# Performance work log

Hardware: AMD Instinct MI355X
Metric: run time of the kernel (lower is better)

The kernel has to match this reference:

```python
import jax, jax.numpy as jnp
import numpy as np

NUM_HEADS = 16
LN_EPS = 1e-5


def setup_inputs() -> dict:
    key = jax.random.key(0)
    ks = jax.random.split(key, 5)
    B, S, E = 4, 1024, 1024
    x = jax.random.normal(ks[0], (B, S, E), dtype=jnp.float32)
    # Linear weights stored torch-style [out, in]; scaled for stable softmax
    Wq = jax.random.normal(ks[1], (E, E), dtype=jnp.float32) * (E ** -0.5)
    Wk = jax.random.normal(ks[2], (E, E), dtype=jnp.float32) * (E ** -0.5)
    Wv = jax.random.normal(ks[3], (E, E), dtype=jnp.float32) * (E ** -0.5)
    Wo = jax.random.normal(ks[4], (E, E), dtype=jnp.float32) * (E ** -0.5)
    gamma = jnp.ones((E,), dtype=jnp.float32)
    beta = jnp.zeros((E,), dtype=jnp.float32)
    return {"x": x, "Wq": Wq, "Wk": Wk, "Wv": Wv, "Wo": Wo, "gamma": gamma, "beta": beta}


def reference(x, Wq, Wk, Wv, Wo, gamma, beta):
    B, S, E = x.shape
    H = NUM_HEADS
    D = E // H
    scale = 1.0 / (D ** 0.5)

    q = x @ Wq.T                      # [B,S,E]
    k = (x @ Wk.T) * scale            # [B,S,E]
    v = x @ Wv.T                      # [B,S,E]

    qh = q.reshape(B, S, H, D)
    kh = k.reshape(B, S, H, D)
    qk = jnp.einsum('bthd,bshd->bhts', qh, kh)        # [B,H,T,S]

    causal = jnp.tril(jnp.ones((S, S), dtype=bool))   # mask==0 -> -inf
    qk = jnp.where(causal, qk, -jnp.inf)
    attn = jax.nn.softmax(qk, axis=-1)                # [B,H,T,S]

    # Faithful to torch.unflatten(v, dim=2, sizes=[-1, num_heads]):
    # heads are the LAST axis of the value split (transposed vs q/k).
    vh = v.reshape(B, S, D, H)                        # [B,S,D,H]
    # einsum 'kjlm,kmij->kiml': out[b,t,h,d] = sum_s vh[b,s,d,h]*attn[b,h,t,s]
    qkv = jnp.einsum('bsdh,bhts->bthd', vh, attn)     # [B,T,H,D]
    qkv = qkv.reshape(B, S, E)

    # LayerNorm over last dim
    mu = jnp.mean(qkv, axis=-1, keepdims=True)
    var = jnp.mean(jnp.square(qkv - mu), axis=-1, keepdims=True)
    ln = (qkv - mu) * jax.lax.rsqrt(var + LN_EPS) * gamma + beta

    return ln @ Wo.T
```

## Files before the change

### kernel.cpp

```cpp
#include <hip/hip_runtime.h>
#include <stdint.h>


using bf16x8 = __attribute__((ext_vector_type(8))) short;
using f32x4  = __attribute__((ext_vector_type(4))) float;
using u16x8  = __attribute__((ext_vector_type(8))) unsigned short;

#define AS1 __attribute__((address_space(1)))
#define AS3 __attribute__((address_space(3)))

__device__ __forceinline__ void gload16(const void* g, void* l) {
  __builtin_amdgcn_global_load_lds((const AS1 uint32_t*)g, (AS3 uint32_t*)l, 16, 0, 0);
}

__device__ __forceinline__ unsigned short f2bf(float f) {
  union { float f; uint32_t u; } v; v.f = f;
  uint32_t u = v.u + 0x7fffu + ((v.u >> 16) & 1u);
  return (unsigned short)(u >> 16);
}
__device__ __forceinline__ float bf2f(unsigned short h) {
  union { uint32_t u; float f; } v; v.u = ((uint32_t)h) << 16;
  return v.f;
}

__global__ __launch_bounds__(256) void cvt_all(const float* __restrict__ x,
                                               const float* __restrict__ Wq,
                                               const float* __restrict__ Wk,
                                               const float* __restrict__ Wv,
                                               const float* __restrict__ Wo,
                                               unsigned short* __restrict__ xb,
                                               unsigned short* __restrict__ wcat,
                                               unsigned short* __restrict__ wob) {
  int i = (int)blockIdx.x * 256 + (int)threadIdx.x;
  const float* src; unsigned short* dst; int off; float scale = 1.0f;
  if (i < 1048576)      { src = x;  dst = xb;             off = i; }
  else if (i < 1310720) { src = Wq; dst = wcat;           off = i - 1048576; }
  else if (i < 1572864) { src = Wk; dst = wcat + 1048576; off = i - 1310720; scale = 0.125f; }
  else if (i < 1835008) { src = Wv; dst = wcat + 2097152; off = i - 1572864; }
  else                  { src = Wo; dst = wob;            off = i - 1835008; }
  float4 v = reinterpret_cast<const float4*>(src)[off];
  ushort4 o;
  o.x = f2bf(v.x * scale);
  o.y = f2bf(v.y * scale);
  o.z = f2bf(v.z * scale);
  o.w = f2bf(v.w * scale);
  reinterpret_cast<ushort4*>(dst)[off] = o;
}

template<int OUTF32>
__global__ __launch_bounds__(256, 2) void gemm_bt(const unsigned short* __restrict__ A,
                                                  const unsigned short* __restrict__ B,
                                                  void* __restrict__ Cv,
                                                  int M, int N, int K) {
  (void)M;
  __shared__ __align__(16) unsigned short lA[128 * 32];
  __shared__ __align__(16) unsigned short lB[128 * 32];
  const int tn_cnt = N >> 7;
  const int nwg = gridDim.x;
  int bid = (int)blockIdx.x;
  int bid2 = (bid & 7) * (nwg >> 3) + (bid >> 3);
  int tm = bid2 / tn_cnt, tn = bid2 % tn_cnt;
  int t = (int)threadIdx.x;
  int w = t >> 6, lane = t & 63, lr = lane & 15, hi = lane >> 4;
  int wr = w >> 1, wc = w & 1;
  int srow = t >> 2, scol = (t & 3) << 3;
  const unsigned short* a0 = A + (size_t)(tm * 128 + srow) * K + scol;
  const unsigned short* a1 = a0 + (size_t)64 * K;
  const unsigned short* b0 = B + (size_t)(tn * 128 + srow) * K + scol;
  const unsigned short* b1 = b0 + (size_t)64 * K;
  char* dA0 = (char*)lA + w * 1024;
  char* dA1 = (char*)lA + 4096 + w * 1024;
  char* dB0 = (char*)lB + w * 1024;
  char* dB1 = (char*)lB + 4096 + w * 1024;
  f32x4 acc[4][4] = {};
  for (int k0 = 0; k0 < K; k0 += 32) {
    __syncthreads();
    gload16(a0 + k0, dA0);
    gload16(a1 + k0, dA1);
    gload16(b0 + k0, dB0);
    gload16(b1 + k0, dB1);
    __syncthreads();
    bf16x8 af[4], bfr[4];
#pragma unroll
    for (int mi = 0; mi < 4; ++mi)
      af[mi] = *reinterpret_cast<const bf16x8*>(&lA[(wr * 64 + mi * 16 + lr) * 32 + hi * 8]);
#pragma unroll
    for (int ni = 0; ni < 4; ++ni)
      bfr[ni] = *reinterpret_cast<const bf16x8*>(&lB[(wc * 64 + ni * 16 + lr) * 32 + hi * 8]);
#pragma unroll
    for (int mi = 0; mi < 4; ++mi)
#pragma unroll
      for (int ni = 0; ni < 4; ++ni)
        acc[mi][ni] = __builtin_amdgcn_mfma_f32_16x16x32_bf16(af[mi], bfr[ni], acc[mi][ni], 0, 0, 0);
  }
#pragma unroll
  for (int mi = 0; mi < 4; ++mi) {
#pragma unroll
    for (int r = 0; r < 4; ++r) {
      size_t row = (size_t)(tm * 128 + wr * 64 + mi * 16 + hi * 4 + r);
#pragma unroll
      for (int ni = 0; ni < 4; ++ni) {
        int col = tn * 128 + wc * 64 + ni * 16 + lr;
        float v = acc[mi][ni][r];
        if (OUTF32) reinterpret_cast<float*>(Cv)[row * N + col] = v;
        else        reinterpret_cast<unsigned short*>(Cv)[row * N + col] = f2bf(v);
      }
    }
  }
}

__global__ __launch_bounds__(256) void vrepack(const unsigned short* __restrict__ QKV,
                                               unsigned short* __restrict__ VhT) {
  __shared__ __align__(16) unsigned short lT[64 * 72];
  int st = (int)blockIdx.x;
  int ct = (int)blockIdx.y;
  int b  = (int)blockIdx.z;
  int t = (int)threadIdx.x;
#pragma unroll
  for (int i = 0; i < 2; ++i) {
    int c = i * 256 + t;
    int row = c >> 3, ch = c & 7;
    u16x8 v = *reinterpret_cast<const u16x8*>(
        QKV + (size_t)(b * 1024 + st * 64 + row) * 3072 + 2048 + ct * 64 + ch * 8);
    *reinterpret_cast<u16x8*>(&lT[row * 72 + ch * 8]) = v;
  }
  __syncthreads();
#pragma unroll
  for (int i = 0; i < 2; ++i) {
    int c2 = i * 256 + t;
    int cl = c2 >> 3, ch = c2 & 7;
    int h = cl & 15;
    int d = ct * 4 + (cl >> 4);
    u16x8 v;
#pragma unroll
    for (int j = 0; j < 8; ++j) v[j] = lT[(ch * 8 + j) * 72 + cl];
    *reinterpret_cast<u16x8*>(
        VhT + (size_t)((b * 16 + h) * 64 + d) * 1024 + st * 64 + ch * 8) = v;
  }
}

__global__ __launch_bounds__(256, 2) void attn_fwd(const unsigned short* __restrict__ QKV,
                                                   const unsigned short* __restrict__ VhT,
                                                   unsigned short* __restrict__ Out) {
  __shared__ __align__(16) unsigned short lQ[128 * 64];
  __shared__ __align__(16) unsigned short lK[2][64 * 64];
  __shared__ __align__(16) unsigned short lV[2][64 * 64];
  __shared__ __align__(16) unsigned short lP[4][32 * 64];
  int bid = (int)blockIdx.x;
  int half = bid >> 8, idx = bid & 255;
  int bh = idx >> 2, jj = idx & 3;
  int qt = half ? jj : 7 - jj;
  int b = bh >> 4, h = bh & 15;
  int t = (int)threadIdx.x;
  int w = t >> 6, lane = t & 63, lr = lane & 15, hi = lane >> 4;
  (void)lane;

  auto stageKV = [&](int kb, int buf) {
#pragma unroll
    for (int i = 0; i < 2; ++i) {
      int c = i * 256 + t;
      int row = c >> 3, slot = c & 7;
      gload16(QKV + (size_t)(b * 1024 + kb * 64 + row) * 3072 + 1024 + h * 64 + ((slot ^ (row & 7)) << 3),
              (char*)lK + buf * 8192 + i * 4096 + w * 1024);
    }
#pragma unroll
    for (int i = 0; i < 2; ++i) {
      int c = i * 256 + t;
      int row = c >> 3, slot = c & 7;
      gload16(VhT + (size_t)(bh * 64 + row) * 1024 + kb * 64 + ((slot ^ (row & 7)) << 3),
              (char*)lV + buf * 8192 + i * 4096 + w * 1024);
    }
  };

#pragma unroll
  for (int i = 0; i < 4; ++i) {
    int c = i * 256 + t;
    int row = c >> 3, slot = c & 7;
    gload16(QKV + (size_t)(b * 1024 + qt * 128 + row) * 3072 + h * 64 + ((slot ^ (row & 7)) << 3),
            (char*)lQ + i * 4096 + w * 1024);
  }
  stageKV(0, 0);
  __syncthreads();

  bf16x8 qfr[2][2];
#pragma unroll
  for (int qf = 0; qf < 2; ++qf)
#pragma unroll
    for (int kc = 0; kc < 2; ++kc) {
      int row = w * 32 + qf * 16 + lr;
      int slot = (kc * 4 + hi) ^ (row & 7);
      qfr[qf][kc] = *reinterpret_cast<const bf16x8*>((const char*)lQ + row * 128 + slot * 16);
    }
  int qbase = qt * 128 + w * 32;
  f32x4 o[2][4] = {};
  float mrun[2][4], lpart[2][4];
#pragma unroll
  for (int qf = 0; qf < 2; ++qf)
#pragma unroll
    for (int r = 0; r < 4; ++r) { mrun[qf][r] = -1e30f; lpart[qf][r] = 0.f; }

  int nkb = 2 * qt + 2;
  for (int kb = 0; kb < nkb; ++kb) {
    int cur = kb & 1;
    if (kb + 1 < nkb) stageKV(kb + 1, cur ^ 1);
    if (kb * 64 <= qbase + 31) {
      const char* kbuf = (const char*)lK + cur * 8192;
      const char* vbuf = (const char*)lV + cur * 8192;
      bf16x8 kfr[4][2];
#pragma unroll
      for (int nf = 0; nf < 4; ++nf)
#pragma unroll
        for (int kc = 0; kc < 2; ++kc) {
          int row = nf * 16 + lr;
          int slot = (kc * 4 + hi) ^ (row & 7);
          kfr[nf][kc] = *reinterpret_cast<const bf16x8*>(kbuf + row * 128 + slot * 16);
        }
      f32x4 s[2][4] = {};
#pragma unroll
      for (int qf = 0; qf < 2; ++qf)
#pragma unroll
        for (int nf = 0; nf < 4; ++nf)
#pragma unroll
          for (int kc = 0; kc < 2; ++kc)
            s[qf][nf] = __builtin_amdgcn_mfma_f32_16x16x32_bf16(qfr[qf][kc], kfr[nf][kc], s[qf][nf], 0, 0, 0);
      bf16x8 vfr[4][2];
#pragma unroll
      for (int df = 0; df < 4; ++df)
#pragma unroll
        for (int kc = 0; kc < 2; ++kc) {
          int row = df * 16 + lr;
          int slot = (kc * 4 + hi) ^ (row & 7);
          vfr[df][kc] = *reinterpret_cast<const bf16x8*>(vbuf + row * 128 + slot * 16);
        }
      if (kb * 64 + 63 > qbase) {
#pragma unroll
        for (int qf = 0; qf < 2; ++qf)
#pragma unroll
          for (int nf = 0; nf < 4; ++nf)
#pragma unroll
            for (int r = 0; r < 4; ++r) {
              int q = qbase + qf * 16 + hi * 4 + r;
              int kv = kb * 64 + nf * 16 + lr;
              if (kv > q) s[qf][nf][r] = -1e30f;
            }
      }
#pragma unroll
      for (int qf = 0; qf < 2; ++qf) {
        float rm[4];
#pragma unroll
        for (int r = 0; r < 4; ++r)
          rm[r] = fmaxf(fmaxf(s[qf][0][r], s[qf][1][r]), fmaxf(s[qf][2][r], s[qf][3][r]));
#pragma unroll
        for (int r = 0; r < 4; ++r) {
          rm[r] = fmaxf(rm[r], __shfl_xor(rm[r], 1));
          rm[r] = fmaxf(rm[r], __shfl_xor(rm[r], 2));
          rm[r] = fmaxf(rm[r], __shfl_xor(rm[r], 4));
          rm[r] = fmaxf(rm[r], __shfl_xor(rm[r], 8));
        }
#pragma unroll
        for (int r = 0; r < 4; ++r) {
          float mn = fmaxf(mrun[qf][r], rm[r]);
          float al = __expf(mrun[qf][r] - mn);
          mrun[qf][r] = mn;
          float ps = 0.f;
#pragma unroll
          for (int nf = 0; nf < 4; ++nf) {
            float p = __expf(s[qf][nf][r] - mn);
            s[qf][nf][r] = p;
            ps += p;
          }
          lpart[qf][r] = lpart[qf][r] * al + ps;
#pragma unroll
          for (int df = 0; df < 4; ++df) o[qf][df][r] *= al;
        }
      }
      char* pb = (char*)lP[w];
#pragma unroll
      for (int qf = 0; qf < 2; ++qf)
#pragma unroll
        for (int nf = 0; nf < 4; ++nf)
#pragma unroll
          for (int r = 0; r < 4; ++r) {
            int rp = qf * 16 + hi * 4 + r;
            int col = nf * 16 + lr;
            int slot = (col >> 3) ^ (rp & 7);
            *reinterpret_cast<unsigned short*>(pb + rp * 128 + slot * 16 + (col & 7) * 2) =
                f2bf(s[qf][nf][r]);
          }
      asm volatile("s_waitcnt lgkmcnt(0)" ::: "memory");
      __builtin_amdgcn_sched_barrier(0);
      bf16x8 pfr[2][2];
#pragma unroll
      for (int qf = 0; qf < 2; ++qf)
#pragma unroll
        for (int kc = 0; kc < 2; ++kc) {
          int row = qf * 16 + lr;
          int slot = (kc * 4 + hi) ^ (row & 7);
          pfr[qf][kc] = *reinterpret_cast<const bf16x8*>(pb + row * 128 + slot * 16);
        }
#pragma unroll
      for (int qf = 0; qf < 2; ++qf)
#pragma unroll
        for (int df = 0; df < 4; ++df)
#pragma unroll
          for (int kc = 0; kc < 2; ++kc)
            o[qf][df] = __builtin_amdgcn_mfma_f32_16x16x32_bf16(pfr[qf][kc], vfr[df][kc], o[qf][df], 0, 0, 0);
    }
    __syncthreads();
  }

#pragma unroll
  for (int qf = 0; qf < 2; ++qf)
#pragma unroll
    for (int r = 0; r < 4; ++r) {
      float l = lpart[qf][r];
      l += __shfl_xor(l, 1);
      l += __shfl_xor(l, 2);
      l += __shfl_xor(l, 4);
      l += __shfl_xor(l, 8);
      float inv = 1.0f / l;
      int qrow = qbase + qf * 16 + hi * 4 + r;
#pragma unroll
      for (int df = 0; df < 4; ++df)
        Out[(size_t)(b * 1024 + qrow) * 1024 + h * 64 + df * 16 + lr] = f2bf(o[qf][df][r] * inv);
    }
}

__global__ __launch_bounds__(256) void lnorm(const unsigned short* __restrict__ X,
                                             unsigned short* __restrict__ Y,
                                             const float* __restrict__ gamma,
                                             const float* __restrict__ beta) {
  int rowi = (int)blockIdx.x * 4 + ((int)threadIdx.x >> 6);
  int lane = (int)threadIdx.x & 63;
  const unsigned short* row = X + (size_t)rowi * 1024;
  u16x8 v0 = reinterpret_cast<const u16x8*>(row)[lane];
  u16x8 v1 = reinterpret_cast<const u16x8*>(row)[lane + 64];
  float f0[8], f1[8];
  float s = 0.f, sq = 0.f;
#pragma unroll
  for (int j = 0; j < 8; ++j) {
    f0[j] = bf2f(v0[j]); f1[j] = bf2f(v1[j]);
    s  += f0[j] + f1[j];
    sq += f0[j] * f0[j] + f1[j] * f1[j];
  }
#pragma unroll
  for (int m = 1; m <= 32; m <<= 1) { s += __shfl_xor(s, m); sq += __shfl_xor(sq, m); }
  float mean = s * (1.0f / 1024.0f);
  float var  = sq * (1.0f / 1024.0f) - mean * mean;
  float rstd = rsqrtf(var + 1e-5f);
  int c0 = lane * 8, c1 = 512 + lane * 8;
  u16x8 o0, o1;
#pragma unroll
  for (int j = 0; j < 8; ++j) {
    o0[j] = f2bf((f0[j] - mean) * rstd * gamma[c0 + j] + beta[c0 + j]);
    o1[j] = f2bf((f1[j] - mean) * rstd * gamma[c1 + j] + beta[c1 + j]);
  }
  reinterpret_cast<u16x8*>(Y + (size_t)rowi * 1024)[lane]      = o0;
  reinterpret_cast<u16x8*>(Y + (size_t)rowi * 1024)[lane + 64] = o1;
}

extern "C" void kernel_launch(void* const* d_in, const int* in_sizes, int n_in,
                              void* d_out, int out_size, void* d_ws, size_t ws_size,
                              hipStream_t stream) {
  (void)in_sizes; (void)n_in; (void)out_size; (void)ws_size;
  const float* x     = (const float*)d_in[0];
  const float* Wq    = (const float*)d_in[1];
  const float* Wk    = (const float*)d_in[2];
  const float* Wv    = (const float*)d_in[3];
  const float* Wo    = (const float*)d_in[4];
  const float* gamma = (const float*)d_in[5];
  const float* beta  = (const float*)d_in[6];
  char* ws = (char*)d_ws;
  unsigned short* xb   = (unsigned short*)(ws);
  unsigned short* wcat = (unsigned short*)(ws + (8u  << 20));
  unsigned short* wob  = (unsigned short*)(ws + (14u << 20));
  unsigned short* qkv  = (unsigned short*)(ws + (16u << 20));
  unsigned short* vht  = (unsigned short*)(ws + (40u << 20));
  unsigned short* att  = (unsigned short*)(ws + (48u << 20));
  unsigned short* lnb  = (unsigned short*)(ws + (56u << 20));

  cvt_all<<<8192, 256, 0, stream>>>(x, Wq, Wk, Wv, Wo, xb, wcat, wob);
  gemm_bt<0><<<768, 256, 0, stream>>>(xb, wcat, qkv, 4096, 3072, 1024);
  vrepack<<<dim3(16, 16, 4), 256, 0, stream>>>(qkv, vht);
  attn_fwd<<<512, 256, 0, stream>>>(qkv, vht, att);
  lnorm<<<1024, 256, 0, stream>>>(att, lnb, gamma, beta);
  gemm_bt<1><<<256, 256, 0, stream>>>(lnb, wob, (void*)d_out, 4096, 1024, 1024);
}
```

Measured before the change: 190.2 us.

## Double-buffer GEMM LDS tiles with K=64 steps and XOR-swizzled layout

```diff
diff --git a/kernel.cpp b/kernel.cpp
--- a/kernel.cpp
+++ b/kernel.cpp
@@ -53,8 +53,8 @@
                                                   void* __restrict__ Cv,
                                                   int M, int N, int K) {
   (void)M;
-  __shared__ __align__(16) unsigned short lA[128 * 32];
-  __shared__ __align__(16) unsigned short lB[128 * 32];
+  __shared__ __align__(16) unsigned short lA[2][128 * 64];
+  __shared__ __align__(16) unsigned short lB[2][128 * 64];
   const int tn_cnt = N >> 7;
   const int nwg = gridDim.x;
   int bid = (int)blockIdx.x;
@@ -63,35 +63,55 @@
   int t = (int)threadIdx.x;
   int w = t >> 6, lane = t & 63, lr = lane & 15, hi = lane >> 4;
   int wr = w >> 1, wc = w & 1;
-  int srow = t >> 2, scol = (t & 3) << 3;
-  const unsigned short* a0 = A + (size_t)(tm * 128 + srow) * K + scol;
-  const unsigned short* a1 = a0 + (size_t)64 * K;
-  const unsigned short* b0 = B + (size_t)(tn * 128 + srow) * K + scol;
-  const unsigned short* b1 = b0 + (size_t)64 * K;
-  char* dA0 = (char*)lA + w * 1024;
-  char* dA1 = (char*)lA + 4096 + w * 1024;
-  char* dB0 = (char*)lB + w * 1024;
-  char* dB1 = (char*)lB + 4096 + w * 1024;
+
+  auto stage = [&](int kt, int buf) {
+#pragma unroll
+    for (int j = 0; j < 4; ++j) {
+      int ch = j * 256 + t;
+      int row = ch >> 3, slot = ch & 7;
+      gload16(A + (size_t)(tm * 128 + row) * K + kt * 64 + ((slot ^ (row & 7)) << 3),
+              (char*)lA[buf] + j * 4096 + w * 1024);
+    }
+#pragma unroll
+    for (int j = 0; j < 4; ++j) {
+      int ch = j * 256 + t;
+      int row = ch >> 3, slot = ch & 7;
+      gload16(B + (size_t)(tn * 128 + row) * K + kt * 64 + ((slot ^ (row & 7)) << 3),
+              (char*)lB[buf] + j * 4096 + w * 1024);
+    }
+  };
+
   f32x4 acc[4][4] = {};
-  for (int k0 = 0; k0 < K; k0 += 32) {
+  stage(0, 0);
+  __syncthreads();
+  const int NT = K >> 6;
+  for (int kt = 0; kt < NT; ++kt) {
+    int cur = kt & 1;
+    if (kt + 1 < NT) stage(kt + 1, cur ^ 1);
+    const char* pa = (const char*)lA[cur];
+    const char* pb = (const char*)lB[cur];
+#pragma unroll
+    for (int kc = 0; kc < 2; ++kc) {
+      bf16x8 af[4], bfr[4];
+#pragma unroll
+      for (int mi = 0; mi < 4; ++mi) {
+        int row = wr * 64 + mi * 16 + lr;
+        int slot = (kc * 4 + hi) ^ (row & 7);
+        af[mi] = *reinterpret_cast<const bf16x8*>(pa + row * 128 + slot * 16);
+      }
+#pragma unroll
+      for (int ni = 0; ni < 4; ++ni) {
+        int row = wc * 64 + ni * 16 + lr;
+        int slot = (kc * 4 + hi) ^ (row & 7);
+        bfr[ni] = *reinterpret_cast<const bf16x8*>(pb + row * 128 + slot * 16);
+      }
+#pragma unroll
+      for (int mi = 0; mi < 4; ++mi)
+#pragma unroll
+        for (int ni = 0; ni < 4; ++ni)
+          acc[mi][ni] = __builtin_amdgcn_mfma_f32_16x16x32_bf16(af[mi], bfr[ni], acc[mi][ni], 0, 0, 0);
+    }
     __syncthreads();
-    gload16(a0 + k0, dA0);
-    gload16(a1 + k0, dA1);
-    gload16(b0 + k0, dB0);
-    gload16(b1 + k0, dB1);
-    __syncthreads();
-    bf16x8 af[4], bfr[4];
-#pragma unroll
-    for (int mi = 0; mi < 4; ++mi)
-      af[mi] = *reinterpret_cast<const bf16x8*>(&lA[(wr * 64 + mi * 16 + lr) * 32 + hi * 8]);
-#pragma unroll
-    for (int ni = 0; ni < 4; ++ni)
-      bfr[ni] = *reinterpret_cast<const bf16x8*>(&lB[(wc * 64 + ni * 16 + lr) * 32 + hi * 8]);
-#pragma unroll
-    for (int mi = 0; mi < 4; ++mi)
-#pragma unroll
-      for (int ni = 0; ni < 4; ++ni)
-        acc[mi][ni] = __builtin_amdgcn_mfma_f32_16x16x32_bf16(af[mi], bfr[ni], acc[mi][ni], 0, 0, 0);
   }
 #pragma unroll
   for (int mi = 0; mi < 4; ++mi) {
```

Measured after the change: 190.7 us. Within noise of the previous version (+0.3%).
